# Performance work log

Measured on AMD Instinct MI355X. Metric: run time of the kernel, lower is better.

The kernel has to match this reference:

```python
import jax, jax.numpy as jnp
import numpy as np

B, S, E, H = 8, 1024, 1024, 16
D = E // H  # head_dim = 64
NEG_INF = jnp.finfo(jnp.float32).min


def setup_inputs() -> dict:
    key = jax.random.key(0)
    ks = jax.random.split(key, 14)
    w = 0.02  # init scale for projection weights
    inp = {
        "query": jax.random.normal(ks[0], (B, S, E), jnp.float32),
        "key": jax.random.normal(ks[1], (B, S, E), jnp.float32),
        "value": jax.random.normal(ks[2], (B, S, E), jnp.float32),
        "attn_bias": jax.random.normal(ks[3], (B, H, S, S), jnp.float32),
        "key_padding_mask": jax.random.randint(ks[4], (B, S), 0, 2).astype(bool),
        "attn_mask": jnp.zeros((S, S), jnp.float32),
        "need_weights": 0,
        "before_softmax": 0,
        "need_head_weights": 0,
        "Wq": jax.random.normal(ks[5], (E, E), jnp.float32) * w,
        "bq": jnp.zeros((E,), jnp.float32),
        "Wk": jax.random.normal(ks[6], (E, E), jnp.float32) * w,
        "bk": jnp.zeros((E,), jnp.float32),
        "Wv": jax.random.normal(ks[7], (E, E), jnp.float32) * w,
        "bv": jnp.zeros((E,), jnp.float32),
        "Wo": jax.random.normal(ks[8], (E, E), jnp.float32) * w,
        "bo": jnp.zeros((E,), jnp.float32),
    }
    return inp


def reference(query, key, value, attn_bias, key_padding_mask, attn_mask,
              need_weights, before_softmax, need_head_weights,
              Wq, bq, Wk, bk, Wv, bv, Wo, bo):
    # self_attention=True: torch code projects q, k, v ALL from `query`.
    scaling = D ** -0.5
    q = (query @ Wq.T + bq) * scaling          # [B,S,E]
    k = query @ Wk.T + bk
    v = query @ Wv.T + bv
    q = q.reshape(B, S, H, D)
    k = k.reshape(B, S, H, D)
    v = v.reshape(B, S, H, D)
    # scores: QK^T + bias + mask, materialized [B,H,S,S] like the torch bmm
    scores = jnp.einsum('bqhd,bkhd->bhqk', q, k)
    scores = scores + attn_bias
    scores = scores + attn_mask[None, None]    # attn_mask broadcast over B,H
    scores = jnp.where(key_padding_mask[:, None, None, :], NEG_INF, scores)
    probs = jax.nn.softmax(scores, axis=-1)    # dropout p=0.0 -> identity
    attn = jnp.einsum('bhqk,bkhd->bqhd', probs, v).reshape(B, S, E)
    out = attn @ Wo.T + bo                     # [B,S,E]
    # need_weights=False path: torch returns (attn, None); return attn only.
    return out
```

## Files before the change

### kernel.cpp

```cpp
#include <hip/hip_runtime.h>

#define B_ 8
#define S_ 1024
#define E_ 1024
#define H_ 16
#define D_ 64

typedef __attribute__((ext_vector_type(8))) short bf16x8;
typedef __attribute__((ext_vector_type(4))) float floatx4;

__device__ __forceinline__ floatx4 mfma16x16x32(bf16x8 a, bf16x8 b, floatx4 c) {
  return __builtin_amdgcn_mfma_f32_16x16x32_bf16(a, b, c, 0, 0, 0);
}

__device__ __forceinline__ unsigned short f2bf(float x) {
  unsigned int u = __builtin_bit_cast(unsigned int, x);
  u += 0x7FFFu + ((u >> 16) & 1u);
  return (unsigned short)(u >> 16);
}

__device__ __forceinline__ void async16(const unsigned short* g, unsigned short* l) {
  __builtin_amdgcn_global_load_lds(
      (const __attribute__((address_space(1))) void*)g,
      (__attribute__((address_space(3))) void*)l, 16, 0, 0);
}

__global__ void mask_prep(const unsigned int* __restrict__ mraw, float* __restrict__ maskadd) {
  __shared__ int flagF, flagB;
  const int tid = threadIdx.x;
  if (tid == 0) { flagF = 0; flagB = 0; }
  __syncthreads();
  int lf = 0, lb = 0;
  for (int i = tid; i < 2048; i += 256) {
    unsigned int v = mraw[i];
    if (v == 0x3F800000u) lf = 1;
    else if (v > 1u) lb = 1;
  }
  if (lf) atomicOr(&flagF, 1);
  if (lb) atomicOr(&flagB, 1);
  __syncthreads();
  const unsigned char* mb = (const unsigned char*)mraw;
  const float* mf = (const float*)mraw;
  const int* mi = (const int*)mraw;
  const int fF = flagF, fB = flagB;
  for (int i = tid; i < B_ * S_; i += 256) {
    int pad;
    if (fF)      pad = (mf[i] != 0.0f);
    else if (fB) pad = (mb[i] != 0);
    else         pad = (mi[i] != 0);
    maskadd[i] = pad ? -3.4028234663852886e38f : 0.0f;
  }
}

__global__ __launch_bounds__(256) void convert_prep(
    const float* __restrict__ q, const float* __restrict__ wq, const float* __restrict__ wk,
    const float* __restrict__ wv, const float* __restrict__ wo,
    unsigned short* __restrict__ xb, unsigned short* __restrict__ wqb,
    unsigned short* __restrict__ wkb, unsigned short* __restrict__ wvb,
    unsigned short* __restrict__ wob)
{
  size_t idx = (size_t)blockIdx.x * 256 + threadIdx.x;
  const float* src; unsigned short* dst; size_t off;
  if (idx < 2097152)      { src = q;  dst = xb;  off = idx; }
  else if (idx < 2359296) { src = wq; dst = wqb; off = idx - 2097152; }
  else if (idx < 2621440) { src = wk; dst = wkb; off = idx - 2359296; }
  else if (idx < 2883584) { src = wv; dst = wvb; off = idx - 2621440; }
  else                    { src = wo; dst = wob; off = idx - 2883584; }
  float4 v = *(const float4*)(src + off * 4);
  ushort4 u; u.x = f2bf(v.x); u.y = f2bf(v.y); u.z = f2bf(v.z); u.w = f2bf(v.w);
  *(ushort4*)(dst + off * 4) = u;
}

__device__ __forceinline__ void gemm_core(
    const unsigned short* __restrict__ A, const unsigned short* __restrict__ Bm,
    int m0, int n0, unsigned short* As, unsigned short* Bs, floatx4 (&acc)[4][4])
{
  const int tid = threadIdx.x;
  const int wave = tid >> 6, lane = tid & 63;
  const int quad = lane >> 4, l16 = lane & 15;
  const int mb = (wave >> 1) * 64, nb = (wave & 1) * 64;
  const int ldrow = lane >> 3;
  const int gchunk = (lane & 7) ^ ldrow;

  for (int ks = 0; ks < 16; ++ks) {
    const int k0 = ks * 64;
    __syncthreads();
    for (int is = 0; is < 4; ++is) {
      int issue = wave * 4 + is;
      async16(A + (size_t)(m0 + issue * 8 + ldrow) * 1024 + k0 + gchunk * 8, &As[issue * 512]);
      async16(Bm + (size_t)(n0 + issue * 8 + ldrow) * 1024 + k0 + gchunk * 8, &Bs[issue * 512]);
    }
    __syncthreads();
    for (int kk = 0; kk < 2; ++kk) {
      const int pc = ((quad + 4 * kk) ^ (l16 & 7)) * 8;
      bf16x8 af[4], bfm[4];
      for (int i = 0; i < 4; ++i)
        af[i] = *(const bf16x8*)(&As[(mb + 16 * i + l16) * 64 + pc]);
      for (int j = 0; j < 4; ++j)
        bfm[j] = *(const bf16x8*)(&Bs[(nb + 16 * j + l16) * 64 + pc]);
      for (int i = 0; i < 4; ++i)
        for (int j = 0; j < 4; ++j)
          acc[i][j] = mfma16x16x32(af[i], bfm[j], acc[i][j]);
    }
  }
}

__global__ __launch_bounds__(256) void gemm_qkv(
    const unsigned short* __restrict__ Xbf,
    const unsigned short* __restrict__ Wqb, const unsigned short* __restrict__ Wkb,
    const unsigned short* __restrict__ Wvb,
    const float* __restrict__ bq, const float* __restrict__ bk, const float* __restrict__ bv,
    unsigned short* __restrict__ qo, unsigned short* __restrict__ ko, unsigned short* __restrict__ vo)
{
  const int tid = threadIdx.x;
  const int flat = blockIdx.y * 24 + blockIdx.x;
  const int swz = (flat & 7) * 192 + (flat >> 3);
  const int bx = swz % 24, by = swz / 24;
  const int n0 = bx * 128;
  const int m0 = by * 128;
  const int which = n0 >> 10;
  const int nn0 = n0 & 1023;
  const unsigned short* W = (which == 0) ? Wqb : (which == 1) ? Wkb : Wvb;
  const float* bias = (which == 0) ? bq : (which == 1) ? bk : bv;

  __shared__ unsigned short smem[128 * 136];
  unsigned short* As = smem;
  unsigned short* Bs = smem + 8192;

  const int lane = tid & 63, wave = tid >> 6;
  const int quad = lane >> 4, l16 = lane & 15;
  const int mb = (wave >> 1) * 64, nb = (wave & 1) * 64;

  floatx4 z = {0.f, 0.f, 0.f, 0.f};
  floatx4 acc[4][4];
  for (int i = 0; i < 4; ++i) for (int j = 0; j < 4; ++j) acc[i][j] = z;

  gemm_core(Xbf, W, m0, nn0, As, Bs, acc);

  float bv4[4];
  for (int j = 0; j < 4; ++j) bv4[j] = bias[nn0 + nb + 16 * j + l16];

  __syncthreads();

  const float scale = (which == 0) ? 0.125f : 1.0f;
  if (which < 2) {
    #pragma unroll
    for (int i = 0; i < 4; ++i)
      #pragma unroll
      for (int r = 0; r < 4; ++r) {
        const int mr = mb + 16 * i + quad * 4 + r;
        #pragma unroll
        for (int j = 0; j < 4; ++j)
          smem[mr * 136 + nb + 16 * j + l16] = f2bf((acc[i][j][r] + bv4[j]) * scale);
      }
  } else {
    #pragma unroll
    for (int i = 0; i < 4; ++i)
      #pragma unroll
      for (int r = 0; r < 4; ++r) {
        const int mr = mb + 16 * i + quad * 4 + r;
        #pragma unroll
        for (int j = 0; j < 4; ++j)
          smem[(nb + 16 * j + l16) * 136 + mr] = f2bf(acc[i][j][r] + bv4[j]);
      }
  }
  __syncthreads();

  const int row = tid >> 1, half = tid & 1;
  if (which < 2) {
    const int m = m0 + row, bb = m >> 10, s = m & 1023;
    const int hh = (nn0 >> 6) + half;
    unsigned short* dst = ((which == 0) ? qo : ko) +
        ((size_t)(bb * 16 + hh) * 1024 + s) * 64;
    #pragma unroll
    for (int c = 0; c < 8; ++c)
      *(bf16x8*)(dst + c * 8) = *(const bf16x8*)(&smem[row * 136 + half * 64 + c * 8]);
  } else {
    const int nglob = nn0 + row;
    const int hh = nglob >> 6, d = nglob & 63;
    const int bb = m0 >> 10;
    unsigned short* dst = vo + ((size_t)(bb * 16 + hh) * 64 + d) * 1024 +
        (m0 & 1023) + half * 64;
    #pragma unroll
    for (int c = 0; c < 8; ++c)
      *(bf16x8*)(dst + c * 8) = *(const bf16x8*)(&smem[row * 136 + half * 64 + c * 8]);
  }
}

__global__ __launch_bounds__(256) void gemm_out(
    const unsigned short* __restrict__ Abf, const unsigned short* __restrict__ Wob,
    const float* __restrict__ bo, float* __restrict__ out)
{
  const int flat = blockIdx.y * 8 + blockIdx.x;
  const int swz = (flat & 7) * 64 + (flat >> 3);
  const int n0 = (swz & 7) * 128;
  const int m0 = (swz >> 3) * 128;
  __shared__ unsigned short As[128 * 64];
  __shared__ unsigned short Bs[128 * 64];

  const int lane = threadIdx.x & 63, wave = threadIdx.x >> 6;
  const int quad = lane >> 4, l16 = lane & 15;
  const int mb = (wave >> 1) * 64, nb = (wave & 1) * 64;

  floatx4 z = {0.f, 0.f, 0.f, 0.f};
  floatx4 acc[4][4];
  for (int i = 0; i < 4; ++i) for (int j = 0; j < 4; ++j) acc[i][j] = z;

  gemm_core(Abf, Wob, m0, n0, As, Bs, acc);

  for (int i = 0; i < 4; ++i) {
    for (int r = 0; r < 4; ++r) {
      int m = m0 + mb + 16 * i + quad * 4 + r;
      for (int j = 0; j < 4; ++j) {
        int n = n0 + nb + 16 * j + l16;
        out[(size_t)m * 1024 + n] = acc[i][j][r] + bo[n];
      }
    }
  }
}

__global__ __launch_bounds__(256) void attn_fwd(
    const unsigned short* __restrict__ qw, const unsigned short* __restrict__ kw,
    const unsigned short* __restrict__ vw, const float* __restrict__ bias,
    const float* __restrict__ amask, const float* __restrict__ maskadd,
    unsigned short* __restrict__ attnw)
{
  const int tid = threadIdx.x;
  const int wave = tid >> 6, lane = tid & 63;
  const int quad = lane >> 4, l16 = lane & 15;
  const int flat = blockIdx.y * 16 + blockIdx.x;
  const int swz = (flat & 7) * 256 + (flat >> 3);
  const int qt = swz & 15, bh = swz >> 4;
  const int b = bh >> 4, h = bh & 15;
  const int qbase = qt * 64 + wave * 16;

  const unsigned short* qh = qw + (size_t)bh * (S_ * D_);
  const unsigned short* kh = kw + (size_t)bh * (S_ * D_);
  const unsigned short* vh = vw + (size_t)bh * (S_ * D_);
  const float* biasb = bias + (size_t)bh * ((size_t)S_ * S_) +
                       (size_t)(qbase + quad * 4) * S_;
  const float* amrow = amask + (size_t)(qbase + quad * 4) * S_;
  const float* madd  = maskadd + b * S_;

  __shared__ unsigned short Vt_all[4][64 * 64];
  __shared__ unsigned short P_all[4][16 * 72];
  unsigned short* Vt = Vt_all[wave];
  unsigned short* Pw = P_all[wave];

  const int srow = lane >> 3;
  const int schk = lane & 7;

  bf16x8 aQ0 = *(const bf16x8*)(qh + (size_t)(qbase + l16) * 64 + quad * 8);
  bf16x8 aQ1 = *(const bf16x8*)(qh + (size_t)(qbase + l16) * 64 + 32 + quad * 8);

  bf16x8 pv[8];

  auto load_v = [&](int key0) {
    #pragma unroll
    for (int i = 0; i < 8; ++i)
      pv[i] = *(const bf16x8*)(vh + (size_t)(srow + 8 * i) * 1024 + key0 + schk * 8);
  };
  auto store_v = [&]() {
    #pragma unroll
    for (int i = 0; i < 8; ++i) {
      const int d = srow + 8 * i;
      *(bf16x8*)(&Vt[d * 64 + ((schk ^ (d & 7)) * 8)]) = pv[i];
    }
  };
  auto load_cinit = [&](int key0, float (&dst)[4][4]) {
    #pragma unroll
    for (int t = 0; t < 4; ++t) {
      const int col = key0 + 16 * t + l16;
      const float mv = madd[col];
      #pragma unroll
      for (int r = 0; r < 4; ++r)
        dst[t][r] = biasb[(size_t)r * S_ + col] + amrow[(size_t)r * S_ + col] + mv;
    }
  };
  auto load_k = [&](int key0, bf16x8 (&K0)[4], bf16x8 (&K1)[4]) {
    #pragma unroll
    for (int t = 0; t < 4; ++t) {
      const unsigned short* kr = kh + (size_t)(key0 + 16 * t + l16) * 64;
      K0[t] = *(const bf16x8*)(kr + quad * 8);
      K1[t] = *(const bf16x8*)(kr + 32 + quad * 8);
    }
  };

  float ccA[4][4], ccB[4][4];
  bf16x8 kA0[4], kA1[4], kB0[4], kB1[4];

  load_v(0); load_cinit(0, ccA); load_k(0, kA0, kA1);
  store_v();
  load_v(64); load_cinit(64, ccB); load_k(64, kB0, kB1);

  floatx4 zz = {0.f, 0.f, 0.f, 0.f};
  floatx4 oacc[4] = {zz, zz, zz, zz};
  float m_run[4], l_run[4];
  for (int r = 0; r < 4; ++r) { m_run[r] = -__builtin_inff(); l_run[r] = 0.f; }

  auto tile_body = [&](int kt, float (&ci)[4][4], bf16x8 (&K0)[4], bf16x8 (&K1)[4]) {
    floatx4 sfr[4];
    #pragma unroll
    for (int t = 0; t < 4; ++t) {
      floatx4 c;
      #pragma unroll
      for (int r = 0; r < 4; ++r) c[r] = ci[t][r];
      c = mfma16x16x32(aQ0, K0[t], c);
      c = mfma16x16x32(aQ1, K1[t], c);
      sfr[t] = c;
    }
    #pragma unroll
    for (int r = 0; r < 4; ++r) {
      float rm = fmaxf(fmaxf(sfr[0][r], sfr[1][r]), fmaxf(sfr[2][r], sfr[3][r]));
      rm = fmaxf(rm, __shfl_xor(rm, 1));
      rm = fmaxf(rm, __shfl_xor(rm, 2));
      rm = fmaxf(rm, __shfl_xor(rm, 4));
      rm = fmaxf(rm, __shfl_xor(rm, 8));
      float mnew = fmaxf(m_run[r], rm);
      float alpha = __expf(m_run[r] - mnew);
      float psum = 0.f;
      #pragma unroll
      for (int t = 0; t < 4; ++t) {
        float p = __expf(sfr[t][r] - mnew);
        psum += p;
        Pw[(quad * 4 + r) * 72 + 16 * t + l16] = f2bf(p);
      }
      psum += __shfl_xor(psum, 1);
      psum += __shfl_xor(psum, 2);
      psum += __shfl_xor(psum, 4);
      psum += __shfl_xor(psum, 8);
      l_run[r] = l_run[r] * alpha + psum;
      m_run[r] = mnew;
      oacc[0][r] *= alpha; oacc[1][r] *= alpha; oacc[2][r] *= alpha; oacc[3][r] *= alpha;
    }
    #pragma unroll
    for (int kc = 0; kc < 2; ++kc) {
      bf16x8 aP = *(const bf16x8*)(Pw + l16 * 72 + kc * 32 + quad * 8);
      const int pc = ((kc * 4 + quad) ^ (l16 & 7)) * 8;
      #pragma unroll
      for (int t = 0; t < 4; ++t) {
        bf16x8 bV = *(const bf16x8*)(&Vt[(16 * t + l16) * 64 + pc]);
        oacc[t] = mfma16x16x32(aP, bV, oacc[t]);
      }
    }
    if (kt < 15) store_v();
    if (kt < 14) {
      load_v((kt + 2) * 64);
      load_cinit((kt + 2) * 64, ci);
      load_k((kt + 2) * 64, K0, K1);
    }
  };

  for (int k2 = 0; k2 < 8; ++k2) {
    tile_body(2 * k2,     ccA, kA0, kA1);
    tile_body(2 * k2 + 1, ccB, kB0, kB1);
  }

  for (int r = 0; r < 4; ++r) {
    int row = qbase + quad * 4 + r;
    float inv = 1.0f / l_run[r];
    unsigned short* orow = attnw + (size_t)(b * S_ + row) * E_ + h * 64;
    for (int t = 0; t < 4; ++t)
      orow[16 * t + l16] = f2bf(oacc[t][r] * inv);
  }
}

extern "C" void kernel_launch(void* const* d_in, const int* in_sizes, int n_in,
                              void* d_out, int out_size, void* d_ws, size_t ws_size,
                              hipStream_t stream) {
  const float* query      = (const float*)d_in[0];
  const float* attn_bias  = (const float*)d_in[3];
  const unsigned int* kpm = (const unsigned int*)d_in[4];
  const float* amask      = (const float*)d_in[5];
  const float* Wq = (const float*)d_in[9];
  const float* bq = (const float*)d_in[10];
  const float* Wk = (const float*)d_in[11];
  const float* bk = (const float*)d_in[12];
  const float* Wv = (const float*)d_in[13];
  const float* bv = (const float*)d_in[14];
  const float* Wo = (const float*)d_in[15];
  const float* bo = (const float*)d_in[16];

  char* ws = (char*)d_ws;
  const size_t MB16 = 16777216;
  unsigned short* qw    = (unsigned short*)(ws);
  unsigned short* kw    = (unsigned short*)(ws + MB16);
  unsigned short* vw    = (unsigned short*)(ws + 2 * MB16);
  unsigned short* xbf   = (unsigned short*)(ws + 3 * MB16);
  unsigned short* attnw = (unsigned short*)(ws + 3 * MB16);
  unsigned short* wqb   = (unsigned short*)(ws + 4 * MB16);
  unsigned short* wkb   = (unsigned short*)(ws + 4 * MB16 + 2097152);
  unsigned short* wvb   = (unsigned short*)(ws + 4 * MB16 + 2 * 2097152);
  unsigned short* wob   = (unsigned short*)(ws + 4 * MB16 + 3 * 2097152);
  float* maskadd        = (float*)(ws + 4 * MB16 + 4 * 2097152);

  mask_prep<<<1, 256, 0, stream>>>(kpm, maskadd);
  convert_prep<<<12288, 256, 0, stream>>>(query, Wq, Wk, Wv, Wo, xbf, wqb, wkb, wvb, wob);
  gemm_qkv<<<dim3(24, 64), 256, 0, stream>>>(xbf, wqb, wkb, wvb, bq, bk, bv, qw, kw, vw);
  attn_fwd<<<dim3(16, 128), 256, 0, stream>>>(qw, kw, vw, attn_bias, amask, maskadd, attnw);
  gemm_out<<<dim3(8, 64), 256, 0, stream>>>(attnw, wob, bo, (float*)d_out);
}
```

Baseline: 1.086 ms.

## Transpose attention MFMA orientation so each lane owns a query row

Swaps the MFMA operand order so the score tile is computed as K·Qᵀ. Each lane then holds one query row's scores across four keys. This lets bias, mask and padding terms load as float4 vectors along the key dimension, and the softmax row reductions shrink to two cross-quad shuffles with a single running max and sum per lane. V is now read directly from global memory as the A operand each tile, replacing the LDS transpose staging. That frees shared memory but issues V global loads inside the tile without prefetch, which may add latency.

Result: slower. 1.116 ms (+2.7%).

```diff
diff --git a/kernel.cpp b/kernel.cpp
--- a/kernel.cpp
+++ b/kernel.cpp
@@ -233,48 +233,32 @@
   const int qt = swz & 15, bh = swz >> 4;
   const int b = bh >> 4, h = bh & 15;
   const int qbase = qt * 64 + wave * 16;
+  const int qrow = qbase + l16;
 
   const unsigned short* qh = qw + (size_t)bh * (S_ * D_);
   const unsigned short* kh = kw + (size_t)bh * (S_ * D_);
   const unsigned short* vh = vw + (size_t)bh * (S_ * D_);
-  const float* biasb = bias + (size_t)bh * ((size_t)S_ * S_) +
-                       (size_t)(qbase + quad * 4) * S_;
-  const float* amrow = amask + (size_t)(qbase + quad * 4) * S_;
+  const float* biasq = bias + (size_t)bh * ((size_t)S_ * S_) + (size_t)qrow * S_;
+  const float* amq   = amask + (size_t)qrow * S_;
   const float* madd  = maskadd + b * S_;
 
-  __shared__ unsigned short Vt_all[4][64 * 64];
   __shared__ unsigned short P_all[4][16 * 72];
-  unsigned short* Vt = Vt_all[wave];
   unsigned short* Pw = P_all[wave];
 
-  const int srow = lane >> 3;
-  const int schk = lane & 7;
-
-  bf16x8 aQ0 = *(const bf16x8*)(qh + (size_t)(qbase + l16) * 64 + quad * 8);
-  bf16x8 aQ1 = *(const bf16x8*)(qh + (size_t)(qbase + l16) * 64 + 32 + quad * 8);
-
-  bf16x8 pv[8];
-
-  auto load_v = [&](int key0) {
-    #pragma unroll
-    for (int i = 0; i < 8; ++i)
-      pv[i] = *(const bf16x8*)(vh + (size_t)(srow + 8 * i) * 1024 + key0 + schk * 8);
-  };
-  auto store_v = [&]() {
-    #pragma unroll
-    for (int i = 0; i < 8; ++i) {
-      const int d = srow + 8 * i;
-      *(bf16x8*)(&Vt[d * 64 + ((schk ^ (d & 7)) * 8)]) = pv[i];
-    }
-  };
-  auto load_cinit = [&](int key0, float (&dst)[4][4]) {
+  bf16x8 bQ0 = *(const bf16x8*)(qh + (size_t)qrow * 64 + quad * 8);
+  bf16x8 bQ1 = *(const bf16x8*)(qh + (size_t)qrow * 64 + 32 + quad * 8);
+
+  auto load_cinit = [&](int key0, float4 (&dst)[4]) {
     #pragma unroll
     for (int t = 0; t < 4; ++t) {
-      const int col = key0 + 16 * t + l16;
-      const float mv = madd[col];
-      #pragma unroll
-      for (int r = 0; r < 4; ++r)
-        dst[t][r] = biasb[(size_t)r * S_ + col] + amrow[(size_t)r * S_ + col] + mv;
+      const int c = key0 + 16 * t + quad * 4;
+      float4 bb = *(const float4*)(biasq + c);
+      float4 aa = *(const float4*)(amq + c);
+      float4 mm = *(const float4*)(madd + c);
+      dst[t].x = bb.x + aa.x + mm.x;
+      dst[t].y = bb.y + aa.y + mm.y;
+      dst[t].z = bb.z + aa.z + mm.z;
+      dst[t].w = bb.w + aa.w + mm.w;
     }
   };
   auto load_k = [&](int key0, bf16x8 (&K0)[4], bf16x8 (&K1)[4]) {
@@ -286,66 +270,71 @@
     }
   };
 
-  float ccA[4][4], ccB[4][4];
+  float4 ccA[4], ccB[4];
   bf16x8 kA0[4], kA1[4], kB0[4], kB1[4];
-
-  load_v(0); load_cinit(0, ccA); load_k(0, kA0, kA1);
-  store_v();
-  load_v(64); load_cinit(64, ccB); load_k(64, kB0, kB1);
+  load_cinit(0, ccA);  load_k(0, kA0, kA1);
+  load_cinit(64, ccB); load_k(64, kB0, kB1);
 
   floatx4 zz = {0.f, 0.f, 0.f, 0.f};
-  floatx4 oacc[4] = {zz, zz, zz, zz};
-  float m_run[4], l_run[4];
-  for (int r = 0; r < 4; ++r) { m_run[r] = -__builtin_inff(); l_run[r] = 0.f; }
-
-  auto tile_body = [&](int kt, float (&ci)[4][4], bf16x8 (&K0)[4], bf16x8 (&K1)[4]) {
+  floatx4 oaccT[4] = {zz, zz, zz, zz};
+  float m_run = -__builtin_inff(), l_run = 0.f;
+
+  auto tile_body = [&](int kt, float4 (&ci)[4], bf16x8 (&K0)[4], bf16x8 (&K1)[4]) {
+    const int key0 = kt * 64;
+    bf16x8 aV0[4], aV1[4];
+    #pragma unroll
+    for (int i = 0; i < 4; ++i) {
+      const unsigned short* vr = vh + (size_t)(16 * i + l16) * 1024 + key0;
+      aV0[i] = *(const bf16x8*)(vr + quad * 8);
+      aV1[i] = *(const bf16x8*)(vr + 32 + quad * 8);
+    }
     floatx4 sfr[4];
     #pragma unroll
     for (int t = 0; t < 4; ++t) {
       floatx4 c;
+      c[0] = ci[t].x; c[1] = ci[t].y; c[2] = ci[t].z; c[3] = ci[t].w;
+      c = mfma16x16x32(K0[t], bQ0, c);
+      c = mfma16x16x32(K1[t], bQ1, c);
+      sfr[t] = c;
+    }
+    float rm = fmaxf(fmaxf(fmaxf(sfr[0][0], sfr[0][1]), fmaxf(sfr[0][2], sfr[0][3])),
+                     fmaxf(fmaxf(sfr[1][0], sfr[1][1]), fmaxf(sfr[1][2], sfr[1][3])));
+    rm = fmaxf(rm, fmaxf(fmaxf(fmaxf(sfr[2][0], sfr[2][1]), fmaxf(sfr[2][2], sfr[2][3])),
+                         fmaxf(fmaxf(sfr[3][0], sfr[3][1]), fmaxf(sfr[3][2], sfr[3][3]))));
+    rm = fmaxf(rm, __shfl_xor(rm, 16));
+    rm = fmaxf(rm, __shfl_xor(rm, 32));
+    const float mnew = fmaxf(m_run, rm);
+    const float alpha = __expf(m_run - mnew);
+    float psum = 0.f;
+    #pragma unroll
+    for (int t = 0; t < 4; ++t) {
+      float p0 = __expf(sfr[t][0] - mnew);
+      float p1 = __expf(sfr[t][1] - mnew);
+      float p2 = __expf(sfr[t][2] - mnew);
+      float p3 = __expf(sfr[t][3] - mnew);
+      psum += (p0 + p1) + (p2 + p3);
+      ushort4 pk;
+      pk.x = f2bf(p0); pk.y = f2bf(p1); pk.z = f2bf(p2); pk.w = f2bf(p3);
+      *(ushort4*)(Pw + l16 * 72 + 16 * t + quad * 4) = pk;
+    }
+    psum += __shfl_xor(psum, 16);
+    psum += __shfl_xor(psum, 32);
+    l_run = l_run * alpha + psum;
+    m_run = mnew;
+    #pragma unroll
+    for (int i = 0; i < 4; ++i) {
+      oaccT[i][0] *= alpha; oaccT[i][1] *= alpha;
+      oaccT[i][2] *= alpha; oaccT[i][3] *= alpha;
+    }
+    #pragma unroll
+    for (int kc = 0; kc < 2; ++kc) {
+      bf16x8 bP = *(const bf16x8*)(Pw + l16 * 72 + kc * 32 + quad * 8);
+      bf16x8* aV = (kc == 0) ? aV0 : aV1;
       #pragma unroll
-      for (int r = 0; r < 4; ++r) c[r] = ci[t][r];
-      c = mfma16x16x32(aQ0, K0[t], c);
-      c = mfma16x16x32(aQ1, K1[t], c);
-      sfr[t] = c;
-    }
-    #pragma unroll
-    for (int r = 0; r < 4; ++r) {
-      float rm = fmaxf(fmaxf(sfr[0][r], sfr[1][r]), fmaxf(sfr[2][r], sfr[3][r]));
-      rm = fmaxf(rm, __shfl_xor(rm, 1));
-      rm = fmaxf(rm, __shfl_xor(rm, 2));
-      rm = fmaxf(rm, __shfl_xor(rm, 4));
-      rm = fmaxf(rm, __shfl_xor(rm, 8));
-      float mnew = fmaxf(m_run[r], rm);
-      float alpha = __expf(m_run[r] - mnew);
-      float psum = 0.f;
-      #pragma unroll
-      for (int t = 0; t < 4; ++t) {
-        float p = __expf(sfr[t][r] - mnew);
-        psum += p;
-        Pw[(quad * 4 + r) * 72 + 16 * t + l16] = f2bf(p);
-      }
-      psum += __shfl_xor(psum, 1);
-      psum += __shfl_xor(psum, 2);
-      psum += __shfl_xor(psum, 4);
-      psum += __shfl_xor(psum, 8);
-      l_run[r] = l_run[r] * alpha + psum;
-      m_run[r] = mnew;
-      oacc[0][r] *= alpha; oacc[1][r] *= alpha; oacc[2][r] *= alpha; oacc[3][r] *= alpha;
-    }
-    #pragma unroll
-    for (int kc = 0; kc < 2; ++kc) {
-      bf16x8 aP = *(const bf16x8*)(Pw + l16 * 72 + kc * 32 + quad * 8);
-      const int pc = ((kc * 4 + quad) ^ (l16 & 7)) * 8;
-      #pragma unroll
-      for (int t = 0; t < 4; ++t) {
-        bf16x8 bV = *(const bf16x8*)(&Vt[(16 * t + l16) * 64 + pc]);
-        oacc[t] = mfma16x16x32(aP, bV, oacc[t]);
-      }
-    }
-    if (kt < 15) store_v();
+      for (int i = 0; i < 4; ++i)
+        oaccT[i] = mfma16x16x32(aV[i], bP, oaccT[i]);
+    }
     if (kt < 14) {
-      load_v((kt + 2) * 64);
       load_cinit((kt + 2) * 64, ci);
       load_k((kt + 2) * 64, K0, K1);
     }
@@ -356,12 +345,16 @@
     tile_body(2 * k2 + 1, ccB, kB0, kB1);
   }
 
-  for (int r = 0; r < 4; ++r) {
-    int row = qbase + quad * 4 + r;
-    float inv = 1.0f / l_run[r];
-    unsigned short* orow = attnw + (size_t)(b * S_ + row) * E_ + h * 64;
-    for (int t = 0; t < 4; ++t)
-      orow[16 * t + l16] = f2bf(oacc[t][r] * inv);
+  const float inv = 1.0f / l_run;
+  unsigned short* orow = attnw + ((size_t)(b * S_) + qrow) * E_ + h * 64;
+  #pragma unroll
+  for (int i = 0; i < 4; ++i) {
+    ushort4 u;
+    u.x = f2bf(oaccT[i][0] * inv);
+    u.y = f2bf(oaccT[i][1] * inv);
+    u.z = f2bf(oaccT[i][2] * inv);
+    u.w = f2bf(oaccT[i][3] * inv);
+    *(ushort4*)(orow + 16 * i + quad * 4) = u;
   }
 }
 
```
